# Kernel tuning notes

Hardware: AMD Instinct MI355X
Metric: run time of the kernel (lower is better)

## Reference

```python
import jax, jax.numpy as jnp
import numpy as np

N = 100000      # nodes
E = 1600000     # edges
F = 128         # num_features
K = 3           # SGConv hops (config.n_layers)
G = 512         # graphs in the batch


def setup_inputs() -> dict:
    key = jax.random.key(0)
    k1, k2, k3, k4 = jax.random.split(key, 4)
    x = jax.random.normal(k1, (N, F), dtype=jnp.float32)
    edge_index = jax.random.randint(k2, (2, E), 0, N, dtype=jnp.int32)
    batch = jnp.sort(jax.random.randint(k3, (N,), 0, G, dtype=jnp.int32))
    W = jax.random.normal(k4, (F, 1), dtype=jnp.float32) * 0.05
    b = jnp.zeros((1,), dtype=jnp.float32)
    return {"x": x, "W": W, "b": b, "edge_index": edge_index, "batch": batch}


def reference(x, W, b, edge_index, batch):
    n = x.shape[0]
    row, col = edge_index[0], edge_index[1]
    # gcn_norm: add self loops, symmetric normalization D^-1/2 (A+I) D^-1/2
    loop = jnp.arange(n, dtype=row.dtype)
    row = jnp.concatenate([row, loop])
    col = jnp.concatenate([col, loop])
    deg = jax.ops.segment_sum(jnp.ones_like(row, dtype=x.dtype), col, num_segments=n)
    dis = jnp.where(deg > 0, jax.lax.rsqrt(deg), 0.0)
    norm = dis[row] * dis[col]  # [E+N]
    # K hops of S @ x (gather from row, scatter-add into col)
    for _ in range(K):
        x = jax.ops.segment_sum(norm[:, None] * x[row], col, num_segments=n)
    out = x @ W + b  # [N, 1]
    # scatter_mean over graph batch vector
    sums = jax.ops.segment_sum(out, batch, num_segments=G)
    cnts = jax.ops.segment_sum(jnp.ones((n,), out.dtype), batch, num_segments=G)
    return sums / jnp.maximum(cnts, 1.0)[:, None]  # [G, 1]
```

## Files before the change

kernel.cpp:

```cpp
#include <hip/hip_runtime.h>


#define BLK 256
#define SB 512
#define CH 8192
#define NBITS 8
#define BSZ 256
#define CAP 6144
#define PSHIFT 20
#define ROWMASK 0xFFFFFu
#define LMAX 512

__global__ __launch_bounds__(BLK) void k_dot(
    const float* __restrict__ x, const float* __restrict__ W,
    int N, int NBUK, float* __restrict__ ydot, unsigned int* __restrict__ gcnt)
{
    int b = blockIdx.x, tid = threadIdx.x;
    if (b == 0)
        for (int j = tid; j < NBUK; j += BLK) gcnt[j] = 0u;
    int l32 = tid & 31;
    float4 wv = ((const float4*)W)[l32];
    int r0 = b * 128;
    int r1 = min(N, r0 + 128);
    for (int r = r0 + (tid >> 5); r < r1; r += BLK / 32) {
        float4 xv = ((const float4*)(x + (size_t)r * 128))[l32];
        float s = xv.x * wv.x + xv.y * wv.y + xv.z * wv.z + xv.w * wv.w;
        #pragma unroll
        for (int o = 16; o; o >>= 1) s += __shfl_xor(s, o, 32);
        if (l32 == 0) ydot[r] = s;
    }
}

__global__ __launch_bounds__(SB) void k_scatter(
    const int* __restrict__ row, const int* __restrict__ col,
    int E, int NBUK, unsigned int* __restrict__ gcnt,
    unsigned int* __restrict__ packed)
{
    __shared__ unsigned int lh[LMAX];
    __shared__ unsigned int lbase[LMAX];
    __shared__ unsigned int lcnt[LMAX];
    int b = blockIdx.x, tid = threadIdx.x;
    for (int j = tid; j < NBUK; j += SB) lh[j] = 0u;
    __syncthreads();
    int s0 = b * CH, s1 = min(E, s0 + CH);
    for (int i = s0 + tid; i < s1; i += SB)
        atomicAdd(&lh[((unsigned int)col[i]) >> NBITS], 1u);
    __syncthreads();
    for (int j = tid; j < NBUK; j += SB) {
        unsigned int c = lh[j];
        lbase[j] = c ? atomicAdd(&gcnt[j], c) : 0u;
        lcnt[j] = 0u;
    }
    __syncthreads();
    for (int i = s0 + tid; i < s1; i += SB) {
        unsigned int c = (unsigned int)col[i];
        unsigned int r = (unsigned int)row[i];
        unsigned int bin = c >> NBITS;
        unsigned int rk = atomicAdd(&lcnt[bin], 1u);
        packed[(size_t)bin * CAP + lbase[bin] + rk] = r | ((c & (BSZ - 1u)) << PSHIFT);
    }
}

__global__ __launch_bounds__(SB) void k_degz0(
    const unsigned int* __restrict__ packed, const unsigned int* __restrict__ gcnt,
    int N, const float* __restrict__ ydot,
    float* __restrict__ rinv, float* __restrict__ rsq, float* __restrict__ z0)
{
    __shared__ unsigned int cnt[BSZ];
    int v = blockIdx.x, tid = threadIdx.x;
    unsigned int S0 = (unsigned int)v * CAP;
    unsigned int S1 = S0 + gcnt[v];
    if (tid < BSZ) cnt[tid] = 0u;
    __syncthreads();
    for (unsigned int i = S0 + tid; i < S1; i += SB)
        atomicAdd(&cnt[packed[i] >> PSHIFT], 1u);
    __syncthreads();
    if (tid < BSZ) {
        int node = (v << NBITS) + tid;
        if (node < N) {
            float d = (float)(cnt[tid] + 1u);
            float rs = rsqrtf(d);
            rinv[node] = 1.0f / d;
            rsq[node] = rs;
            z0[node] = rs * ydot[node];
        }
    }
}

__global__ __launch_bounds__(SB) void k_hop(
    const unsigned int* __restrict__ packed, const unsigned int* __restrict__ gcnt,
    int N, const float* __restrict__ coef,
    const float* __restrict__ zin, float* __restrict__ zout)
{
    __shared__ float acc[BSZ];
    int v = blockIdx.x, tid = threadIdx.x;
    unsigned int S0 = (unsigned int)v * CAP;
    unsigned int S1 = S0 + gcnt[v];
    if (tid < BSZ) acc[tid] = 0.f;
    __syncthreads();
    unsigned int i = S0 + tid;
    for (; i + 7u * SB < S1; i += 8u * SB) {
        unsigned int p0 = packed[i];
        unsigned int p1 = packed[i + SB];
        unsigned int p2 = packed[i + 2u * SB];
        unsigned int p3 = packed[i + 3u * SB];
        unsigned int p4 = packed[i + 4u * SB];
        unsigned int p5 = packed[i + 5u * SB];
        unsigned int p6 = packed[i + 6u * SB];
        unsigned int p7 = packed[i + 7u * SB];
        float a0 = zin[p0 & ROWMASK];
        float a1 = zin[p1 & ROWMASK];
        float a2 = zin[p2 & ROWMASK];
        float a3 = zin[p3 & ROWMASK];
        float a4 = zin[p4 & ROWMASK];
        float a5 = zin[p5 & ROWMASK];
        float a6 = zin[p6 & ROWMASK];
        float a7 = zin[p7 & ROWMASK];
        atomicAdd(&acc[p0 >> PSHIFT], a0);
        atomicAdd(&acc[p1 >> PSHIFT], a1);
        atomicAdd(&acc[p2 >> PSHIFT], a2);
        atomicAdd(&acc[p3 >> PSHIFT], a3);
        atomicAdd(&acc[p4 >> PSHIFT], a4);
        atomicAdd(&acc[p5 >> PSHIFT], a5);
        atomicAdd(&acc[p6 >> PSHIFT], a6);
        atomicAdd(&acc[p7 >> PSHIFT], a7);
    }
    for (; i < S1; i += SB) {
        unsigned int p = packed[i];
        atomicAdd(&acc[p >> PSHIFT], zin[p & ROWMASK]);
    }
    __syncthreads();
    if (tid < BSZ) {
        int node = (v << NBITS) + tid;
        if (node < N) zout[node] = (zin[node] + acc[tid]) * coef[node];
    }
}

__global__ __launch_bounds__(BLK) void k_seg(
    const float* __restrict__ y, const int* __restrict__ batch,
    const float* __restrict__ bias, int N, int G, float* __restrict__ out)
{
    int wave = blockIdx.x * (BLK / 64) + (threadIdx.x >> 6);
    int lane = threadIdx.x & 63;
    if (wave >= G) return;
    int lo = 0, hi = N;
    while (lo < hi) { int m = (lo + hi) >> 1; if (batch[m] < wave) lo = m + 1; else hi = m; }
    int s0 = lo;
    lo = s0; hi = N;
    while (lo < hi) { int m = (lo + hi) >> 1; if (batch[m] < wave + 1) lo = m + 1; else hi = m; }
    int s1 = lo;
    float sum = 0.f;
    for (int i = s0 + lane; i < s1; i += 64) sum += y[i];
    #pragma unroll
    for (int o = 32; o; o >>= 1) sum += __shfl_xor(sum, o);
    if (lane == 0) {
        int cnt = s1 - s0;
        out[wave] = (cnt > 0) ? (sum / (float)cnt + bias[0]) : 0.f;
    }
}

extern "C" void kernel_launch(void* const* d_in, const int* in_sizes, int n_in,
                              void* d_out, int out_size, void* d_ws, size_t ws_size,
                              hipStream_t stream) {
    const float* x     = (const float*)d_in[0];
    const float* W     = (const float*)d_in[1];
    const float* bias  = (const float*)d_in[2];
    const int*   ei    = (const int*)d_in[3];
    const int*   batch = (const int*)d_in[4];
    float* out = (float*)d_out;

    const int N = in_sizes[0] / 128;
    const int E = in_sizes[3] / 2;
    const int G = out_size;

    const int* row = ei;
    const int* col = ei + E;

    const int NBUK = (N + BSZ - 1) / BSZ;
    const int NB   = (E + CH - 1) / CH;
    const int NDOT = (N + 127) / 128;

    char* w = (char*)d_ws;
    unsigned int* gcnt   = (unsigned int*)w;  w += (size_t)NBUK * 4;
    unsigned int* packed = (unsigned int*)w;  w += (size_t)NBUK * CAP * 4;
    float* ydot = (float*)w;  w += (size_t)N * 4;
    float* rinv = (float*)w;  w += (size_t)N * 4;
    float* rsq  = (float*)w;  w += (size_t)N * 4;
    float* z0   = (float*)w;  w += (size_t)N * 4;
    float* z1   = (float*)w;

    k_dot<<<NDOT, BLK, 0, stream>>>(x, W, N, NBUK, ydot, gcnt);
    k_scatter<<<NB, SB, 0, stream>>>(row, col, E, NBUK, gcnt, packed);
    k_degz0<<<NBUK, SB, 0, stream>>>(packed, gcnt, N, ydot, rinv, rsq, z0);
    k_hop<<<NBUK, SB, 0, stream>>>(packed, gcnt, N, rinv, z0, z1);
    k_hop<<<NBUK, SB, 0, stream>>>(packed, gcnt, N, rinv, z1, z0);
    k_hop<<<NBUK, SB, 0, stream>>>(packed, gcnt, N, rsq, z0, z1);
    k_seg<<<(G + (BLK / 64) - 1) / (BLK / 64), BLK, 0, stream>>>(z1, batch, bias, N, G, out);
}
```

Baseline: 179.1 us.

## Replace global-atomic bucketing with per-chunk fixed slots and fuse dot into scatter

Each edge chunk now writes into its own fixed region of 64 slots per destination bucket, prefilled with a sentinel. This removes the histogram pass and the global atomic offset reservation. The x·W dot product is folded into the same launch as extra blocks, which drops one kernel launch. The degree and hop kernels walk every chunk's slot range and skip sentinels. The cost is a much larger packed buffer with mostly-empty slots, so more memory is written and re-read on every hop, and edges are silently dropped if a chunk puts more than 64 edges into one bucket.

```diff
diff --git a/kernel.cpp b/kernel.cpp
--- a/kernel.cpp
+++ b/kernel.cpp
@@ -6,74 +6,68 @@
 #define CH 8192
 #define NBITS 8
 #define BSZ 256
-#define CAP 6144
+#define SLOTC 64
 #define PSHIFT 20
 #define ROWMASK 0xFFFFFu
+#define SENT 0xFFFFFFFFu
 #define LMAX 512
 
-__global__ __launch_bounds__(BLK) void k_dot(
+__global__ __launch_bounds__(SB) void k_dot_scatter(
     const float* __restrict__ x, const float* __restrict__ W,
-    int N, int NBUK, float* __restrict__ ydot, unsigned int* __restrict__ gcnt)
+    const int* __restrict__ row, const int* __restrict__ col,
+    int N, int E, int NB, int NBUK,
+    unsigned int* __restrict__ packed,
+    float* __restrict__ ydot)
 {
     int b = blockIdx.x, tid = threadIdx.x;
-    if (b == 0)
-        for (int j = tid; j < NBUK; j += BLK) gcnt[j] = 0u;
-    int l32 = tid & 31;
-    float4 wv = ((const float4*)W)[l32];
-    int r0 = b * 128;
-    int r1 = min(N, r0 + 128);
-    for (int r = r0 + (tid >> 5); r < r1; r += BLK / 32) {
-        float4 xv = ((const float4*)(x + (size_t)r * 128))[l32];
-        float s = xv.x * wv.x + xv.y * wv.y + xv.z * wv.z + xv.w * wv.w;
-        #pragma unroll
-        for (int o = 16; o; o >>= 1) s += __shfl_xor(s, o, 32);
-        if (l32 == 0) ydot[r] = s;
-    }
-}
-
-__global__ __launch_bounds__(SB) void k_scatter(
-    const int* __restrict__ row, const int* __restrict__ col,
-    int E, int NBUK, unsigned int* __restrict__ gcnt,
-    unsigned int* __restrict__ packed)
-{
-    __shared__ unsigned int lh[LMAX];
-    __shared__ unsigned int lbase[LMAX];
-    __shared__ unsigned int lcnt[LMAX];
-    int b = blockIdx.x, tid = threadIdx.x;
-    for (int j = tid; j < NBUK; j += SB) lh[j] = 0u;
-    __syncthreads();
-    int s0 = b * CH, s1 = min(E, s0 + CH);
-    for (int i = s0 + tid; i < s1; i += SB)
-        atomicAdd(&lh[((unsigned int)col[i]) >> NBITS], 1u);
-    __syncthreads();
-    for (int j = tid; j < NBUK; j += SB) {
-        unsigned int c = lh[j];
-        lbase[j] = c ? atomicAdd(&gcnt[j], c) : 0u;
-        lcnt[j] = 0u;
-    }
-    __syncthreads();
-    for (int i = s0 + tid; i < s1; i += SB) {
-        unsigned int c = (unsigned int)col[i];
-        unsigned int r = (unsigned int)row[i];
-        unsigned int bin = c >> NBITS;
-        unsigned int rk = atomicAdd(&lcnt[bin], 1u);
-        packed[(size_t)bin * CAP + lbase[bin] + rk] = r | ((c & (BSZ - 1u)) << PSHIFT);
+    if (b < NB) {
+        __shared__ unsigned int lcnt[LMAX];
+        unsigned int* reg = packed + (size_t)b * NBUK * SLOTC;
+        for (int j = tid; j < NBUK; j += SB) lcnt[j] = 0u;
+        int tot = NBUK * SLOTC;
+        for (int j = tid; j < tot; j += SB) reg[j] = SENT;
+        __syncthreads();
+        int s0 = b * CH, s1 = min(E, s0 + CH);
+        for (int i = s0 + tid; i < s1; i += SB) {
+            unsigned int c = (unsigned int)col[i];
+            unsigned int r = (unsigned int)row[i];
+            unsigned int bin = c >> NBITS;
+            unsigned int rk = atomicAdd(&lcnt[bin], 1u);
+            if (rk < SLOTC)
+                reg[bin * SLOTC + rk] = r | ((c & (BSZ - 1u)) << PSHIFT);
+        }
+    } else {
+        int rb = b - NB;
+        int l32 = tid & 31;
+        float4 wv = ((const float4*)W)[l32];
+        int r0 = rb * 256;
+        int r1 = min(N, r0 + 256);
+        for (int r = r0 + (tid >> 5); r < r1; r += SB / 32) {
+            float4 xv = ((const float4*)(x + (size_t)r * 128))[l32];
+            float s = xv.x * wv.x + xv.y * wv.y + xv.z * wv.z + xv.w * wv.w;
+            #pragma unroll
+            for (int o = 16; o; o >>= 1) s += __shfl_xor(s, o, 32);
+            if (l32 == 0) ydot[r] = s;
+        }
     }
 }
 
 __global__ __launch_bounds__(SB) void k_degz0(
-    const unsigned int* __restrict__ packed, const unsigned int* __restrict__ gcnt,
-    int N, const float* __restrict__ ydot,
+    const unsigned int* __restrict__ packed, int NB, int NBUK, int N,
+    const float* __restrict__ ydot,
     float* __restrict__ rinv, float* __restrict__ rsq, float* __restrict__ z0)
 {
     __shared__ unsigned int cnt[BSZ];
     int v = blockIdx.x, tid = threadIdx.x;
-    unsigned int S0 = (unsigned int)v * CAP;
-    unsigned int S1 = S0 + gcnt[v];
+    unsigned int rowstride = (unsigned int)NBUK * SLOTC;
+    unsigned int vbase = (unsigned int)v * SLOTC;
+    unsigned int total = (unsigned int)NB * SLOTC;
     if (tid < BSZ) cnt[tid] = 0u;
     __syncthreads();
-    for (unsigned int i = S0 + tid; i < S1; i += SB)
-        atomicAdd(&cnt[packed[i] >> PSHIFT], 1u);
+    for (unsigned int j = tid; j < total; j += SB) {
+        unsigned int p = packed[(size_t)(j >> 6) * rowstride + vbase + (j & 63u)];
+        if (p != SENT) atomicAdd(&cnt[p >> PSHIFT], 1u);
+    }
     __syncthreads();
     if (tid < BSZ) {
         int node = (v << NBITS) + tid;
@@ -88,47 +82,50 @@
 }
 
 __global__ __launch_bounds__(SB) void k_hop(
-    const unsigned int* __restrict__ packed, const unsigned int* __restrict__ gcnt,
-    int N, const float* __restrict__ coef,
+    const unsigned int* __restrict__ packed, int NB, int NBUK, int N,
+    const float* __restrict__ coef,
     const float* __restrict__ zin, float* __restrict__ zout)
 {
     __shared__ float acc[BSZ];
     int v = blockIdx.x, tid = threadIdx.x;
-    unsigned int S0 = (unsigned int)v * CAP;
-    unsigned int S1 = S0 + gcnt[v];
+    unsigned int rowstride = (unsigned int)NBUK * SLOTC;
+    unsigned int vbase = (unsigned int)v * SLOTC;
+    unsigned int total = (unsigned int)NB * SLOTC;
     if (tid < BSZ) acc[tid] = 0.f;
     __syncthreads();
-    unsigned int i = S0 + tid;
-    for (; i + 7u * SB < S1; i += 8u * SB) {
-        unsigned int p0 = packed[i];
-        unsigned int p1 = packed[i + SB];
-        unsigned int p2 = packed[i + 2u * SB];
-        unsigned int p3 = packed[i + 3u * SB];
-        unsigned int p4 = packed[i + 4u * SB];
-        unsigned int p5 = packed[i + 5u * SB];
-        unsigned int p6 = packed[i + 6u * SB];
-        unsigned int p7 = packed[i + 7u * SB];
-        float a0 = zin[p0 & ROWMASK];
-        float a1 = zin[p1 & ROWMASK];
-        float a2 = zin[p2 & ROWMASK];
-        float a3 = zin[p3 & ROWMASK];
-        float a4 = zin[p4 & ROWMASK];
-        float a5 = zin[p5 & ROWMASK];
-        float a6 = zin[p6 & ROWMASK];
-        float a7 = zin[p7 & ROWMASK];
-        atomicAdd(&acc[p0 >> PSHIFT], a0);
-        atomicAdd(&acc[p1 >> PSHIFT], a1);
-        atomicAdd(&acc[p2 >> PSHIFT], a2);
-        atomicAdd(&acc[p3 >> PSHIFT], a3);
-        atomicAdd(&acc[p4 >> PSHIFT], a4);
-        atomicAdd(&acc[p5 >> PSHIFT], a5);
-        atomicAdd(&acc[p6 >> PSHIFT], a6);
-        atomicAdd(&acc[p7 >> PSHIFT], a7);
+    unsigned int j = tid;
+    #define ADDR(jj) ((size_t)((jj) >> 6) * rowstride + vbase + ((jj) & 63u))
+    for (; j + 7u * SB < total; j += 8u * SB) {
+        unsigned int p0 = packed[ADDR(j)];
+        unsigned int p1 = packed[ADDR(j + SB)];
+        unsigned int p2 = packed[ADDR(j + 2u * SB)];
+        unsigned int p3 = packed[ADDR(j + 3u * SB)];
+        unsigned int p4 = packed[ADDR(j + 4u * SB)];
+        unsigned int p5 = packed[ADDR(j + 5u * SB)];
+        unsigned int p6 = packed[ADDR(j + 6u * SB)];
+        unsigned int p7 = packed[ADDR(j + 7u * SB)];
+        float a0 = (p0 != SENT) ? zin[p0 & ROWMASK] : 0.f;
+        float a1 = (p1 != SENT) ? zin[p1 & ROWMASK] : 0.f;
+        float a2 = (p2 != SENT) ? zin[p2 & ROWMASK] : 0.f;
+        float a3 = (p3 != SENT) ? zin[p3 & ROWMASK] : 0.f;
+        float a4 = (p4 != SENT) ? zin[p4 & ROWMASK] : 0.f;
+        float a5 = (p5 != SENT) ? zin[p5 & ROWMASK] : 0.f;
+        float a6 = (p6 != SENT) ? zin[p6 & ROWMASK] : 0.f;
+        float a7 = (p7 != SENT) ? zin[p7 & ROWMASK] : 0.f;
+        if (p0 != SENT) atomicAdd(&acc[p0 >> PSHIFT], a0);
+        if (p1 != SENT) atomicAdd(&acc[p1 >> PSHIFT], a1);
+        if (p2 != SENT) atomicAdd(&acc[p2 >> PSHIFT], a2);
+        if (p3 != SENT) atomicAdd(&acc[p3 >> PSHIFT], a3);
+        if (p4 != SENT) atomicAdd(&acc[p4 >> PSHIFT], a4);
+        if (p5 != SENT) atomicAdd(&acc[p5 >> PSHIFT], a5);
+        if (p6 != SENT) atomicAdd(&acc[p6 >> PSHIFT], a6);
+        if (p7 != SENT) atomicAdd(&acc[p7 >> PSHIFT], a7);
     }
-    for (; i < S1; i += SB) {
-        unsigned int p = packed[i];
-        atomicAdd(&acc[p >> PSHIFT], zin[p & ROWMASK]);
+    for (; j < total; j += SB) {
+        unsigned int p = packed[ADDR(j)];
+        if (p != SENT) atomicAdd(&acc[p >> PSHIFT], zin[p & ROWMASK]);
     }
+    #undef ADDR
     __syncthreads();
     if (tid < BSZ) {
         int node = (v << NBITS) + tid;
@@ -178,22 +175,21 @@
 
     const int NBUK = (N + BSZ - 1) / BSZ;
     const int NB   = (E + CH - 1) / CH;
-    const int NDOT = (N + 127) / 128;
+    const int NDOT = (N + 255) / 256;
 
     char* w = (char*)d_ws;
-    unsigned int* gcnt   = (unsigned int*)w;  w += (size_t)NBUK * 4;
-    unsigned int* packed = (unsigned int*)w;  w += (size_t)NBUK * CAP * 4;
+    unsigned int* packed = (unsigned int*)w;  w += (size_t)NB * NBUK * SLOTC * 4;
     float* ydot = (float*)w;  w += (size_t)N * 4;
     float* rinv = (float*)w;  w += (size_t)N * 4;
     float* rsq  = (float*)w;  w += (size_t)N * 4;
     float* z0   = (float*)w;  w += (size_t)N * 4;
     float* z1   = (float*)w;
 
-    k_dot<<<NDOT, BLK, 0, stream>>>(x, W, N, NBUK, ydot, gcnt);
-    k_scatter<<<NB, SB, 0, stream>>>(row, col, E, NBUK, gcnt, packed);
-    k_degz0<<<NBUK, SB, 0, stream>>>(packed, gcnt, N, ydot, rinv, rsq, z0);
-    k_hop<<<NBUK, SB, 0, stream>>>(packed, gcnt, N, rinv, z0, z1);
-    k_hop<<<NBUK, SB, 0, stream>>>(packed, gcnt, N, rinv, z1, z0);
-    k_hop<<<NBUK, SB, 0, stream>>>(packed, gcnt, N, rsq, z0, z1);
+    k_dot_scatter<<<NB + NDOT, SB, 0, stream>>>(x, W, row, col, N, E, NB, NBUK,
+                                                packed, ydot);
+    k_degz0<<<NBUK, SB, 0, stream>>>(packed, NB, NBUK, N, ydot, rinv, rsq, z0);
+    k_hop<<<NBUK, SB, 0, stream>>>(packed, NB, NBUK, N, rinv, z0, z1);
+    k_hop<<<NBUK, SB, 0, stream>>>(packed, NB, NBUK, N, rinv, z1, z0);
+    k_hop<<<NBUK, SB, 0, stream>>>(packed, NB, NBUK, N, rsq, z0, z1);
     k_seg<<<(G + (BLK / 64) - 1) / (BLK / 64), BLK, 0, stream>>>(z1, batch, bias, N, G, out);
 }
```

New measurement: 183.2 us. 1.02x slower.
